# Performance work log

Measured on AMD Instinct MI355X. Metric: run time of the kernel, lower is better.

The kernel has to match this reference:

```python
import jax, jax.numpy as jnp
import numpy as np


def setup_inputs() -> dict:
    key = jax.random.key(0)
    k1, k2 = jax.random.split(key)
    tensor_1 = jax.random.normal(k1, (8192, 256), dtype=jnp.float32)
    tensor_2 = jax.random.normal(k2, (16384, 256), dtype=jnp.float32)
    return {"tensor_1": tensor_1, "tensor_2": tensor_2}


def reference(tensor_1, tensor_2):
    # L2-normalize along the feature dim (matches torch .norm(dim=-1), no eps)
    n1 = tensor_1 / jnp.linalg.norm(tensor_1, axis=-1, keepdims=True)  # [N, d]
    n2 = tensor_2 / jnp.linalg.norm(tensor_2, axis=-1, keepdims=True)  # [M, d]
    cos_sim = jnp.einsum("nd,md->nm", n1, n2)  # [N, M] cosine similarity
    top3, _ = jax.lax.top_k(cos_sim, 3)        # [N, 3]
    return top3.mean(axis=-1)                  # [N]
```

## Files before the change

### kernel.cpp

```cpp
#include <hip/hip_runtime.h>
#include <hip/hip_bf16.h>
#include <stdint.h>

#define N1 8192
#define N2 16384
#define DIM 256
#define NSPLIT 16
#define BM 128
#define BN 128
#define BK 64
#define COLS_PER_SPLIT (N2 / NSPLIT)
#define NT_PER_SPLIT (COLS_PER_SPLIT / BN)
#define NPART (NSPLIT * 2)

typedef short v8s  __attribute__((ext_vector_type(8)));
typedef float f32x4 __attribute__((ext_vector_type(4)));

#define GLD16(g, l)                                                                         \
  __builtin_amdgcn_global_load_lds((const __attribute__((address_space(1))) uint32_t*)(g),  \
                                   (__attribute__((address_space(3))) uint32_t*)(l), 16, 0, 0)

__device__ __forceinline__ void top3_insert(float v, float& t0, float& t1, float& t2) {
    float nt1 = __builtin_amdgcn_fmed3f(v, t0, t1);
    float nt2 = __builtin_amdgcn_fmed3f(v, t1, t2);
    t0 = fmaxf(t0, v);
    t1 = nt1;
    t2 = nt2;
}

__global__ __launch_bounds__(256) void normalize_kernel(
        const float* __restrict__ inA, const float* __restrict__ inB,
        __hip_bfloat16* __restrict__ outA, __hip_bfloat16* __restrict__ outB) {
    const int gw   = blockIdx.x * 4 + (threadIdx.x >> 6);
    const int lane = threadIdx.x & 63;
    const float* in;
    __hip_bfloat16* out;
    int row;
    if (gw < N1) { in = inA; out = outA; row = gw; }
    else         { in = inB; out = outB; row = gw - N1; }
    const float4 v = *(const float4*)(in + (size_t)row * DIM + lane * 4);
    float s = v.x * v.x + v.y * v.y + v.z * v.z + v.w * v.w;
    #pragma unroll
    for (int off = 32; off; off >>= 1) s += __shfl_xor(s, off, 64);
    const float inv = 1.0f / sqrtf(s);
    __hip_bfloat16 o[4];
    o[0] = __float2bfloat16(v.x * inv);
    o[1] = __float2bfloat16(v.y * inv);
    o[2] = __float2bfloat16(v.z * inv);
    o[3] = __float2bfloat16(v.w * inv);
    *(uint2*)(out + (size_t)row * DIM + lane * 4) = *(uint2*)o;
}

__global__ __launch_bounds__(256, 2) void gemm_top3_kernel(
        const __hip_bfloat16* __restrict__ A, const __hip_bfloat16* __restrict__ B,
        float* __restrict__ partial) {
    __shared__ char smem[16384 + 16384];
    char* tileA = smem;
    char* tileB = smem + 16384;

    const int tid  = threadIdx.x;
    const int wave = tid >> 6;
    const int lane = tid & 63;
    const int lo   = lane & 15;
    const int quad = lane >> 4;
    const int rb    = blockIdx.x >> 4;
    const int split = blockIdx.x & 15;
    const int row0 = rb * BM;
    const int C0   = split * COLS_PER_SPLIT;
    const int wr = (wave >> 1) * 64;
    const int wc = (wave & 1) * 64;

    const int lr = lane >> 3;
    const int s8 = lane & 7;
    const int sx = s8 ^ lr;

    const char* Agbase = (const char*)A + ((size_t)(row0 + wave * 32 + lr)) * 512 + sx * 16;
    const char* Bgbase = (const char*)B + ((size_t)(C0   + wave * 32 + lr)) * 512 + sx * 16;
    char* AldsBase = tileA + wave * 32 * 128;
    char* BldsBase = tileB + wave * 32 * 128;

    int aoff[2], boff[2];
    #pragma unroll
    for (int ks = 0; ks < 2; ks++) {
        const int swz = ((ks * 4 + quad) ^ (lo & 7)) * 16;
        aoff[ks] = (wr + lo) * 128 + swz;
        boff[ks] = (wc + lo) * 128 + swz;
    }

    float t0[16], t1[16], t2[16];
    #pragma unroll
    for (int i = 0; i < 16; i++) { t0[i] = -1e30f; t1[i] = -1e30f; t2[i] = -1e30f; }

    for (int nt = 0; nt < NT_PER_SPLIT; ++nt) {
        f32x4 acc[4][4];
        #pragma unroll
        for (int kk = 0; kk < 4; kk++) {
            __syncthreads();
            #pragma unroll
            for (int j = 0; j < 4; j++)
                GLD16(Agbase + (size_t)j * 4096 + kk * 128, AldsBase + j * 1024);
            #pragma unroll
            for (int j = 0; j < 4; j++)
                GLD16(Bgbase + (size_t)nt * 65536 + (size_t)j * 4096 + kk * 128,
                      BldsBase + j * 1024);
            __syncthreads();
            #pragma unroll
            for (int ks = 0; ks < 2; ks++) {
                v8s af[4];
                #pragma unroll
                for (int rt = 0; rt < 4; rt++)
                    af[rt] = *(const v8s*)(tileA + aoff[ks] + rt * 2048);
                #pragma unroll
                for (int ct = 0; ct < 4; ct++) {
                    v8s bf = *(const v8s*)(tileB + boff[ks] + ct * 2048);
                    #pragma unroll
                    for (int rt = 0; rt < 4; rt++) {
                        if (kk == 0 && ks == 0)
                            acc[rt][ct] = __builtin_amdgcn_mfma_f32_16x16x32_bf16(
                                af[rt], bf, (f32x4){0.f, 0.f, 0.f, 0.f}, 0, 0, 0);
                        else
                            acc[rt][ct] = __builtin_amdgcn_mfma_f32_16x16x32_bf16(
                                af[rt], bf, acc[rt][ct], 0, 0, 0);
                    }
                }
            }
        }
        #pragma unroll
        for (int rt = 0; rt < 4; rt++)
            #pragma unroll
            for (int r = 0; r < 4; r++) {
                const int i = rt * 4 + r;
                #pragma unroll
                for (int ct = 0; ct < 4; ct++)
                    top3_insert(acc[rt][ct][r], t0[i], t1[i], t2[i]);
            }
    }

    #pragma unroll
    for (int step = 1; step < 16; step <<= 1) {
        #pragma unroll
        for (int i = 0; i < 16; i++) {
            float b0 = __shfl_xor(t0[i], step, 64);
            float b1 = __shfl_xor(t1[i], step, 64);
            float b2 = __shfl_xor(t2[i], step, 64);
            top3_insert(b0, t0[i], t1[i], t2[i]);
            top3_insert(b1, t0[i], t1[i], t2[i]);
            top3_insert(b2, t0[i], t1[i], t2[i]);
        }
    }

    if (lo == 0) {
        #pragma unroll
        for (int rt = 0; rt < 4; rt++)
            #pragma unroll
            for (int r = 0; r < 4; r++) {
                const int i = rt * 4 + r;
                const int row = row0 + wr + rt * 16 + quad * 4 + r;
                float* p = partial + ((size_t)row * NPART + (split * 2 + (wave & 1))) * 3;
                p[0] = t0[i]; p[1] = t1[i]; p[2] = t2[i];
            }
    }
}

__global__ __launch_bounds__(256) void merge_kernel(
        const float* __restrict__ partial, float* __restrict__ out) {
    const int row = blockIdx.x * 256 + threadIdx.x;
    if (row >= N1) return;
    const float* p = partial + (size_t)row * NPART * 3;
    float t0 = -1e30f, t1 = -1e30f, t2 = -1e30f;
    #pragma unroll
    for (int i = 0; i < NPART * 3; i++) top3_insert(p[i], t0, t1, t2);
    out[row] = (t0 + t1 + t2) * (1.0f / 3.0f);
}

extern "C" void kernel_launch(void* const* d_in, const int* in_sizes, int n_in,
                              void* d_out, int out_size, void* d_ws, size_t ws_size,
                              hipStream_t stream) {
    const float* tA = (const float*)d_in[0];
    const float* tB = (const float*)d_in[1];
    float* out = (float*)d_out;

    __hip_bfloat16* An = (__hip_bfloat16*)d_ws;
    __hip_bfloat16* Bn = An + (size_t)N1 * DIM;
    float* partial = (float*)(Bn + (size_t)N2 * DIM);

    normalize_kernel<<<(N1 + N2) / 4, 256, 0, stream>>>(tA, tB, An, Bn);
    gemm_top3_kernel<<<(N1 / BM) * NSPLIT, 256, 0, stream>>>(An, Bn, partial);
    merge_kernel<<<N1 / 256, 256, 0, stream>>>(partial, out);
}
```

Before: 158.8 us.

## Double-buffer LDS tiles to overlap global loads with MFMA compute

Doubles the shared-memory tile area into two ping-pong buffers. Each k-step now issues the async global-to-LDS loads for the next step into the other buffer before running MFMAs on the current one. This replaces two barriers per step with one and is meant to hide global load latency behind compute. In exchange, LDS per block doubles to 64KB, and the compiler may still insert conservative vmcnt waits before LDS reads, which would limit the overlap.

```diff
diff --git a/kernel.cpp b/kernel.cpp
--- a/kernel.cpp
+++ b/kernel.cpp
@@ -54,9 +54,7 @@
 __global__ __launch_bounds__(256, 2) void gemm_top3_kernel(
         const __hip_bfloat16* __restrict__ A, const __hip_bfloat16* __restrict__ B,
         float* __restrict__ partial) {
-    __shared__ char smem[16384 + 16384];
-    char* tileA = smem;
-    char* tileB = smem + 16384;
+    __shared__ char smem[2 * 32768];
 
     const int tid  = threadIdx.x;
     const int wave = tid >> 6;
@@ -76,8 +74,7 @@
 
     const char* Agbase = (const char*)A + ((size_t)(row0 + wave * 32 + lr)) * 512 + sx * 16;
     const char* Bgbase = (const char*)B + ((size_t)(C0   + wave * 32 + lr)) * 512 + sx * 16;
-    char* AldsBase = tileA + wave * 32 * 128;
-    char* BldsBase = tileB + wave * 32 * 128;
+    const int ldsWaveOff = wave * 32 * 128;
 
     int aoff[2], boff[2];
     #pragma unroll
@@ -91,28 +88,43 @@
     #pragma unroll
     for (int i = 0; i < 16; i++) { t0[i] = -1e30f; t1[i] = -1e30f; t2[i] = -1e30f; }
 
+    #define STAGE(nt_, kk_, buf_)                                                     \
+        do {                                                                          \
+            char* Al = smem + (buf_) * 32768 + ldsWaveOff;                            \
+            char* Bl = smem + (buf_) * 32768 + 16384 + ldsWaveOff;                    \
+            _Pragma("unroll")                                                         \
+            for (int j = 0; j < 4; j++)                                               \
+                GLD16(Agbase + (size_t)j * 4096 + (kk_) * 128, Al + j * 1024);        \
+            _Pragma("unroll")                                                         \
+            for (int j = 0; j < 4; j++)                                               \
+                GLD16(Bgbase + (size_t)(nt_) * 65536 + (size_t)j * 4096 + (kk_) * 128,\
+                      Bl + j * 1024);                                                 \
+        } while (0)
+
+    STAGE(0, 0, 0);
+
     for (int nt = 0; nt < NT_PER_SPLIT; ++nt) {
         f32x4 acc[4][4];
         #pragma unroll
         for (int kk = 0; kk < 4; kk++) {
+            const int buf = kk & 1;
             __syncthreads();
-            #pragma unroll
-            for (int j = 0; j < 4; j++)
-                GLD16(Agbase + (size_t)j * 4096 + kk * 128, AldsBase + j * 1024);
-            #pragma unroll
-            for (int j = 0; j < 4; j++)
-                GLD16(Bgbase + (size_t)nt * 65536 + (size_t)j * 4096 + kk * 128,
-                      BldsBase + j * 1024);
-            __syncthreads();
+            if (kk < 3) {
+                STAGE(nt, kk + 1, buf ^ 1);
+            } else if (nt < NT_PER_SPLIT - 1) {
+                STAGE(nt + 1, 0, buf ^ 1);
+            }
+            const char* tA = smem + buf * 32768;
+            const char* tB = smem + buf * 32768 + 16384;
             #pragma unroll
             for (int ks = 0; ks < 2; ks++) {
                 v8s af[4];
                 #pragma unroll
                 for (int rt = 0; rt < 4; rt++)
-                    af[rt] = *(const v8s*)(tileA + aoff[ks] + rt * 2048);
+                    af[rt] = *(const v8s*)(tA + aoff[ks] + rt * 2048);
                 #pragma unroll
                 for (int ct = 0; ct < 4; ct++) {
-                    v8s bf = *(const v8s*)(tileB + boff[ks] + ct * 2048);
+                    v8s bf = *(const v8s*)(tB + boff[ks] + ct * 2048);
                     #pragma unroll
                     for (int rt = 0; rt < 4; rt++) {
                         if (kk == 0 && ks == 0)
```

New measurement: 155.6 us. 1.02x faster.
